# Optimization experiments

Hardware: AMD Instinct MI355X
Metric: run time of the kernel (lower is better)

Reference implementation:

```python
import jax, jax.numpy as jnp
import numpy as np

D_NODE, D_EDGE, D_MODEL, TOPK, N_HEADS = 64, 16, 256, 5, 4
HEAD_DIM = D_MODEL // N_HEADS


def setup_inputs() -> dict:
    key = jax.random.key(0)
    ks = jax.random.split(key, 24)
    B, N = 256, 512
    E = N - 1
    def lin(k, fi, fo):
        k1, k2 = jax.random.split(k)
        s = 1.0 / np.sqrt(fi)
        return (jax.random.uniform(k1, (fi, fo), jnp.float32, -s, s),
                jax.random.uniform(k2, (fo,), jnp.float32, -s, s))
    Wn, bn = lin(ks[0], 8, D_NODE)
    We, be = lin(ks[1], 3, D_EDGE)
    Wq, bq = lin(ks[2], D_NODE, D_MODEL)
    Wkv, bkv = lin(ks[3], 2 * D_NODE + D_EDGE, 2 * D_MODEL)
    # MultiheadAttention in/out projections (fixed shared weights)
    Wiq, biq = lin(ks[4], D_MODEL, D_MODEL)
    Wik, bik = lin(ks[5], D_MODEL, D_MODEL)
    Wiv, biv = lin(ks[6], D_MODEL, D_MODEL)
    Wo, bo = lin(ks[7], D_MODEL, D_MODEL)
    Wf1, bf1 = lin(ks[8], D_NODE + D_MODEL, D_MODEL)
    Wf2, bf2 = lin(ks[9], D_MODEL, D_MODEL)
    Ws1, bs1 = lin(ks[10], D_NODE + D_EDGE + D_MODEL, D_MODEL)
    Ws2, bs2 = lin(ks[11], D_MODEL, 1 + 6 * D_MODEL)
    node_raw = jax.random.normal(ks[12], (B, N, 8), jnp.float32)
    edge_raw = jax.random.normal(ks[13], (B, E, 3), jnp.float32)
    return dict(node_raw=node_raw, edge_raw=edge_raw, ego_id=0,
                Wn=Wn, bn=bn, We=We, be=be, Wq=Wq, bq=bq, Wkv=Wkv, bkv=bkv,
                Wiq=Wiq, biq=biq, Wik=Wik, bik=bik, Wiv=Wiv, biv=biv,
                Wo=Wo, bo=bo, Wf1=Wf1, bf1=bf1, Wf2=Wf2, bf2=bf2,
                Ws1=Ws1, bs1=bs1, Ws2=Ws2, bs2=bs2)


def reference(node_raw, edge_raw, ego_id,
              Wn, bn, We, be, Wq, bq, Wkv, bkv,
              Wiq, biq, Wik, bik, Wiv, biv, Wo, bo,
              Wf1, bf1, Wf2, bf2, Ws1, bs1, Ws2, bs2):
    B, N, _ = node_raw.shape
    E = N - 1
    ego_id = int(ego_id)
    idx = np.arange(N)
    neighbor_idx = jnp.asarray(idx[idx != ego_id])  # (E,)

    node_feat = node_raw @ Wn + bn                   # (B, N, d_node)
    edge_feat = edge_raw @ We + be                   # (B, E, d_edge)
    ego_feat = node_feat[:, ego_id]                  # (B, d_node)
    neighbor_feat = node_feat[:, neighbor_idx]       # (B, E, d_node)

    ego_bcast = jnp.broadcast_to(ego_feat[:, None, :], (B, E, D_NODE))
    edge_input = jnp.concatenate([ego_bcast, edge_feat, neighbor_feat], -1)

    Q = ego_feat @ Wq + bq                           # (B, d_model)
    kv = edge_input @ Wkv + bkv                      # (B, E, 2*d_model)
    K, V = kv[..., :D_MODEL], kv[..., D_MODEL:]

    # MultiheadAttention: single query per batch, E keys/values
    q = (Q @ Wiq + biq).reshape(B, N_HEADS, HEAD_DIM)
    k = (K @ Wik + bik).reshape(B, E, N_HEADS, HEAD_DIM)
    v = (V @ Wiv + biv).reshape(B, E, N_HEADS, HEAD_DIM)
    scores = jnp.einsum('bhd,behd->bhe', q, k) / np.sqrt(HEAD_DIM)
    attn = jax.nn.softmax(scores, axis=-1)           # (B, H, E)
    ctx = jnp.einsum('bhe,behd->bhd', attn, v).reshape(B, D_MODEL)
    c_ego = ctx @ Wo + bo                            # (B, d_model)

    h = jnp.concatenate([ego_feat, c_ego], -1)
    h_ego_prime = jax.nn.relu(h @ Wf1 + bf1) @ Wf2 + bf2  # (B, d_model)

    c_bcast = jnp.broadcast_to(c_ego[:, None, :], (B, E, D_MODEL))
    edge_input2 = jnp.concatenate([neighbor_feat, edge_feat, c_bcast], -1)
    score_out = jax.nn.relu(edge_input2 @ Ws1 + bs1) @ Ws2 + bs2  # (B,E,1+6*dm)
    score = score_out[..., 0]                        # (B, E)
    h_enc = score_out[..., 1:].reshape(B, E, 6, D_MODEL)

    topk_val, topk_idx = jax.lax.top_k(score, TOPK)  # (B, topk)
    selected = jnp.take_along_axis(h_enc, topk_idx[:, :, None, None], axis=1)
    alpha = jax.nn.softmax(topk_val, axis=-1)[:, :, None, None]  # (B,topk,1,1)
    selected = selected * alpha
    return h_ego_prime, selected, topk_idx, alpha
```

## Files before the change

kernel.cpp:

```cpp
#include <hip/hip_runtime.h>
#include <hip/hip_bf16.h>
#include <math.h>

constexpr int B = 256, NN = 512, EE = 511;

constexpr size_t F_NF    = 0;
constexpr size_t F_EF    = F_NF   + (size_t)B*NN*64;
constexpr size_t F_WCK   = F_EF   + (size_t)B*EE*16;
constexpr size_t F_BCK   = F_WCK  + 144*256;
constexpr size_t F_WCV   = F_BCK  + 256;
constexpr size_t F_BCV   = F_WCV  + 144*256;
constexpr size_t F_WQ2   = F_BCV  + 256;
constexpr size_t F_BQ2   = F_WQ2  + 64*256;
constexpr size_t F_Q     = F_BQ2  + 256;
constexpr size_t F_AW    = F_Q    + (size_t)B*256;
constexpr size_t F_C0    = F_AW   + (size_t)B*4*80;
constexpr size_t F_SC    = F_C0   + (size_t)B*4;
constexpr size_t F_US    = F_SC   + (size_t)B*4*EE;
constexpr size_t F_CEGO  = F_US   + (size_t)B*4*80;
constexpr size_t F_CVEC  = F_CEGO + (size_t)B*256;
constexpr size_t F_SC2   = F_CVEC + (size_t)B*256;
constexpr size_t F_ALPHA = F_SC2  + (size_t)B*EE;
constexpr size_t F_TKI   = F_ALPHA+ (size_t)B*5;
constexpr size_t F_HS    = F_SC;

constexpr size_t O_HEGO  = 0;
constexpr size_t O_SEL   = 65536;
constexpr size_t O_TKI   = 2031616;
constexpr size_t O_ALPHA = 2032896;

__global__ void k_fuse(const float* Wkv, const float* bkv, const float* Wik, const float* bik,
                       const float* Wiv, const float* biv, const float* Wq,  const float* bq,
                       const float* Wiq, const float* biq, float* ws){
  int t = blockIdx.x*256 + threadIdx.x;
  if (t < 36864){
    int r = t >> 8, c = t & 255;
    float a = 0.f;
    for (int m=0;m<256;m++) a += Wkv[(size_t)r*512+m] * Wik[(size_t)m*256+c];
    ws[F_WCK + t] = a;
  } else if (t < 37120){
    int c = t - 36864;
    float a = bik[c];
    for (int m=0;m<256;m++) a += bkv[m] * Wik[(size_t)m*256+c];
    ws[F_BCK + c] = a;
  } else if (t < 73984){
    int i = t - 37120; int r = i >> 8, c = i & 255;
    float a = 0.f;
    for (int m=0;m<256;m++) a += Wkv[(size_t)r*512+256+m] * Wiv[(size_t)m*256+c];
    ws[F_WCV + i] = a;
  } else if (t < 74240){
    int c = t - 73984;
    float a = biv[c];
    for (int m=0;m<256;m++) a += bkv[256+m] * Wiv[(size_t)m*256+c];
    ws[F_BCV + c] = a;
  } else if (t < 90624){
    int i = t - 74240; int r = i >> 8, c = i & 255;
    float a = 0.f;
    for (int m=0;m<256;m++) a += Wq[(size_t)r*256+m] * Wiq[(size_t)m*256+c];
    ws[F_WQ2 + i] = a;
  } else if (t < 90880){
    int c = t - 90624;
    float a = biq[c];
    for (int m=0;m<256;m++) a += bq[m] * Wiq[(size_t)m*256+c];
    ws[F_BQ2 + c] = a;
  }
}

__global__ void k_nf(const float* node_raw, const float* Wn, const float* bn, float* ws){
  size_t t = (size_t)blockIdx.x*256 + threadIdx.x;
  int j = (int)(t & 63); size_t row = t >> 6;
  float a = bn[j];
  #pragma unroll
  for (int i=0;i<8;i++) a += node_raw[row*8+i] * Wn[(size_t)i*64+j];
  ws[F_NF + t] = a;
}

__global__ void k_ef(const float* edge_raw, const float* We, const float* be, float* ws){
  size_t t = (size_t)blockIdx.x*256 + threadIdx.x;
  int j = (int)(t & 15); size_t row = t >> 4;
  float a = be[j];
  #pragma unroll
  for (int i=0;i<3;i++) a += edge_raw[row*3+i] * We[(size_t)i*16+j];
  ws[F_EF + t] = a;
}

__global__ void k_head(const int* ego_p, float* ws){
  int b = blockIdx.x >> 2, h = blockIdx.x & 3;
  int tid = threadIdx.x;
  __shared__ float qh[64];
  __shared__ float red[256];
  int ego = *ego_p;
  const float* egf = ws + F_NF + ((size_t)b*NN+ego)*64;
  if (tid < 64){
    int c = h*64 + tid;
    float a = ws[F_BQ2 + c];
    for (int i=0;i<64;i++) a += egf[i]*ws[F_WQ2 + (size_t)i*256 + c];
    qh[tid] = a;
  }
  __syncthreads();
  const float* Wck = ws + F_WCK;
  float p = 0.f;
  size_t awbase = F_AW + ((size_t)(b*4+h))*80;
  if (tid < 64){
    const float* wr = Wck + (size_t)(80+tid)*256 + h*64;
    float a=0.f; for(int d=0;d<64;d++) a += wr[d]*qh[d];
    ws[awbase + tid] = a;
  } else if (tid < 80){
    int i = tid-64;
    const float* wr = Wck + (size_t)(64+i)*256 + h*64;
    float a=0.f; for(int d=0;d<64;d++) a += wr[d]*qh[d];
    ws[awbase + 64 + i] = a;
  } else if (tid < 144){
    int j = tid-80;
    const float* wr = Wck + (size_t)j*256 + h*64;
    float a=0.f; for(int d=0;d<64;d++) a += wr[d]*qh[d];
    p = egf[j] * a;
  } else if (tid < 208){
    int d = tid-144;
    p = ws[F_BCK + h*64 + d] * qh[d];
  }
  red[tid]=p; __syncthreads();
  for (int s=128;s>0;s>>=1){ if(tid<s) red[tid]+=red[tid+s]; __syncthreads(); }
  if (tid==0) ws[F_C0 + b*4 + h] = red[0];
}

__global__ void k_scores(const int* ego_p, float* ws){
  int tile = blockIdx.x, b = blockIdx.y, tid = threadIdx.x;
  __shared__ float awz[4][80];
  __shared__ float c0s[4];
  for (int l=tid; l<320; l+=256) awz[l/80][l%80] = ws[F_AW + (size_t)b*320 + l];
  if (tid<4) c0s[tid] = ws[F_C0 + b*4 + tid];
  __syncthreads();
  int e = tile*256 + tid;
  if (e >= EE) return;
  int ego = *ego_p;
  int node = e < ego ? e : e+1;
  const float4* nr = (const float4*)(ws + F_NF + ((size_t)b*NN+node)*64);
  const float4* er = (const float4*)(ws + F_EF + ((size_t)b*EE+e)*16);
  float s[4] = {c0s[0],c0s[1],c0s[2],c0s[3]};
  #pragma unroll
  for (int i=0;i<16;i++){
    float4 x = nr[i];
    #pragma unroll
    for (int h=0;h<4;h++)
      s[h] += x.x*awz[h][i*4] + x.y*awz[h][i*4+1] + x.z*awz[h][i*4+2] + x.w*awz[h][i*4+3];
  }
  #pragma unroll
  for (int i=0;i<4;i++){
    float4 x = er[i];
    #pragma unroll
    for (int h=0;h<4;h++)
      s[h] += x.x*awz[h][64+i*4] + x.y*awz[h][64+i*4+1] + x.z*awz[h][64+i*4+2] + x.w*awz[h][64+i*4+3];
  }
  #pragma unroll
  for (int h=0;h<4;h++) ws[F_SC + ((size_t)(b*4+h))*EE + e] = s[h]*0.125f;
}

__global__ void k_attn(const int* ego_p, float* ws){
  int bh = blockIdx.x; int b = bh>>2; int tid = threadIdx.x;
  __shared__ float sc[512];
  __shared__ float red[256];
  const float* s = ws + F_SC + (size_t)bh*EE;
  float v0 = tid<EE ? s[tid] : -INFINITY;
  float v1 = (tid+256)<EE ? s[tid+256] : -INFINITY;
  red[tid] = fmaxf(v0,v1); __syncthreads();
  for (int st=128;st>0;st>>=1){ if(tid<st) red[tid]=fmaxf(red[tid],red[tid+st]); __syncthreads(); }
  float m = red[0]; __syncthreads();
  float e0 = tid<EE ? expf(v0-m) : 0.f;
  float e1 = (tid+256)<EE ? expf(v1-m) : 0.f;
  red[tid] = e0+e1; __syncthreads();
  for (int st=128;st>0;st>>=1){ if(tid<st) red[tid]+=red[tid+st]; __syncthreads(); }
  float inv = 1.f/red[0];
  sc[tid] = e0*inv;
  sc[tid+256] = e1*inv;
  __syncthreads();
  int ego = *ego_p;
  if (tid < 64){
    const float* base = ws + F_NF + (size_t)b*NN*64 + tid;
    float a = 0.f;
    for (int e=0;e<EE;e++){
      int node = e<ego?e:e+1;
      a += sc[e]*base[(size_t)node*64];
    }
    ws[F_US + (size_t)bh*80 + tid] = a;
  } else if (tid < 80){
    int d = tid-64;
    const float* base = ws + F_EF + (size_t)b*EE*16 + d;
    float a = 0.f;
    for (int e=0;e<EE;e++) a += sc[e]*base[(size_t)e*16];
    ws[F_US + (size_t)bh*80 + tid] = a;
  }
}

__global__ void k_bfinal(const int* ego_p,
                         const float* Wo, const float* bo,
                         const float* Wf1, const float* bf1p,
                         const float* Wf2, const float* bf2p,
                         const float* Ws1, const float* bs1,
                         float* ws, float* out){
  int b = blockIdx.x, t = threadIdx.x;
  __shared__ float ego_s[64], us_s[4][80], ctx_s[256], cego_s[256], hf_s[256];
  int ego = *ego_p;
  if (t < 64) ego_s[t] = ws[F_NF + ((size_t)b*NN+ego)*64 + t];
  for (int l=t; l<320; l+=256) us_s[l/80][l%80] = ws[F_US + (size_t)b*320 + l];
  __syncthreads();
  {
    int h = t >> 6;
    const float* Wcv = ws + F_WCV;
    float a = ws[F_BCV + t];
    for (int i=0;i<64;i++) a += ego_s[i]*Wcv[(size_t)i*256+t];
    for (int i=0;i<16;i++) a += us_s[h][64+i]*Wcv[(size_t)(64+i)*256+t];
    for (int i=0;i<64;i++) a += us_s[h][i]*Wcv[(size_t)(80+i)*256+t];
    ctx_s[t]=a;
  }
  __syncthreads();
  {
    float a = bo[t];
    for (int i=0;i<256;i++) a += ctx_s[i]*Wo[(size_t)i*256+t];
    cego_s[t]=a; ws[F_CEGO + (size_t)b*256+t]=a;
  }
  __syncthreads();
  {
    float a = bf1p[t];
    for (int i=0;i<64;i++)  a += ego_s[i]*Wf1[(size_t)i*256+t];
    for (int i=0;i<256;i++) a += cego_s[i]*Wf1[(size_t)(64+i)*256+t];
    hf_s[t]=fmaxf(a,0.f);
  }
  __syncthreads();
  {
    float a = bf2p[t];
    for (int i=0;i<256;i++) a += hf_s[i]*Wf2[(size_t)i*256+t];
    out[O_HEGO + (size_t)b*256+t] = a;
  }
  {
    float a = bs1[t];
    for (int i=0;i<256;i++) a += cego_s[i]*Ws1[(size_t)(80+i)*256+t];
    ws[F_CVEC + (size_t)b*256+t]=a;
  }
}

__global__ __launch_bounds__(512) void k_bigscore(const int* ego_p, const float* Ws1,
                                                  const float* Ws2, const float* bs2, float* ws){
  int tile = blockIdx.x, b = blockIdx.y;
  int tid = threadIdx.x;
  __shared__ float Fe[64][80];
  __shared__ float Bs[16][256];
  __shared__ float cv_s[256], w2_s[256];
  int ego = *ego_p;
  if (tid < 256){
    cv_s[tid] = ws[F_CVEC + (size_t)b*256 + tid];
    w2_s[tid] = Ws2[(size_t)tid*1537];
  }
  for (int l=tid; l<80*64; l+=512){
    int e = l/80, k = l - e*80;
    int eg = tile*64 + e;
    float v = 0.f;
    if (eg < EE){
      int node = eg<ego?eg:eg+1;
      v = (k<64) ? ws[F_NF + ((size_t)b*NN+node)*64 + k]
                 : ws[F_EF + ((size_t)b*EE+eg)*16 + (k-64)];
    }
    Fe[e][k] = v;
  }
  int tc = tid & 31, te = tid >> 5;
  float acc[4][8];
  #pragma unroll
  for (int i=0;i<4;i++)
    #pragma unroll
    for (int j=0;j<8;j++) acc[i][j]=0.f;

  for (int c=0;c<5;c++){
    __syncthreads();
    {
      float4* dst = (float4*)&Bs[0][0];
      const float4* s4 = (const float4*)(Ws1 + (size_t)(c*16)*256);
      dst[tid]       = s4[tid];
      dst[tid + 512] = s4[tid + 512];
    }
    __syncthreads();
    #pragma unroll
    for (int kk=0; kk<16; kk+=4){
      float A[4][4];
      #pragma unroll
      for (int i=0;i<4;i++){
        float4 t4 = *(const float4*)&Fe[te*4+i][c*16+kk];
        A[i][0]=t4.x; A[i][1]=t4.y; A[i][2]=t4.z; A[i][3]=t4.w;
      }
      #pragma unroll
      for (int q=0;q<4;q++){
        float4 b0 = *(const float4*)&Bs[kk+q][tc*4];
        float4 b1 = *(const float4*)&Bs[kk+q][128 + tc*4];
        float bw[8] = {b0.x,b0.y,b0.z,b0.w,b1.x,b1.y,b1.z,b1.w};
        #pragma unroll
        for (int i=0;i<4;i++)
          #pragma unroll
          for (int j=0;j<8;j++) acc[i][j] = fmaf(A[i][q], bw[j], acc[i][j]);
      }
    }
  }
  float bs20 = bs2[0];
  #pragma unroll
  for (int i=0;i<4;i++){
    float p = 0.f;
    #pragma unroll
    for (int j=0;j<4;j++){
      int col = tc*4 + j;
      float hcol = acc[i][j] + cv_s[col];
      p += fmaxf(hcol,0.f)*w2_s[col];
    }
    #pragma unroll
    for (int j=0;j<4;j++){
      int col = 128 + tc*4 + j;
      float hcol = acc[i][4+j] + cv_s[col];
      p += fmaxf(hcol,0.f)*w2_s[col];
    }
    #pragma unroll
    for (int m=16;m>0;m>>=1) p += __shfl_xor(p, m, 64);
    if (tc==0){
      int eg = tile*64 + te*4 + i;
      if (eg < EE) ws[F_SC2 + (size_t)b*EE + eg] = p + bs20;
    }
  }
}

__global__ void k_topk(float* ws, float* out){
  int b = blockIdx.x, tid = threadIdx.x;
  __shared__ float sv[256]; __shared__ int si[256];
  __shared__ float tv[8];   __shared__ int tix[8];
  const float* s = ws + F_SC2 + (size_t)b*EE;
  float v0 = tid<EE ? s[tid] : -INFINITY;       int i0 = tid;
  float v1 = (tid+256)<EE ? s[tid+256] : -INFINITY; int i1 = tid+256;
  for (int t=0;t<5;t++){
    float bvv; int bii;
    if (v0 > v1 || (v0==v1 && i0<i1)){ bvv=v0; bii=i0; } else { bvv=v1; bii=i1; }
    sv[tid]=bvv; si[tid]=bii; __syncthreads();
    for (int st=128; st>0; st>>=1){
      if (tid<st){
        float ov=sv[tid+st]; int oi=si[tid+st];
        if (ov > sv[tid] || (ov==sv[tid] && oi<si[tid])){ sv[tid]=ov; si[tid]=oi; }
      }
      __syncthreads();
    }
    if (tid==0){ tv[t]=sv[0]; tix[t]=si[0]; }
    __syncthreads();
    int w = tix[t];
    if (i0==w) v0=-INFINITY;
    if (i1==w) v1=-INFINITY;
    __syncthreads();
  }
  if (tid==0){
    float m = tv[0];
    float ex[5]; float sum=0.f;
    for (int t=0;t<5;t++){ ex[t]=expf(tv[t]-m); sum+=ex[t]; }
    for (int t=0;t<5;t++){
      float al = ex[t]/sum;
      ws[F_ALPHA + (size_t)b*5+t] = al;
      ((int*)(ws + F_TKI))[b*5+t] = tix[t];
      out[O_TKI   + (size_t)b*5+t] = (float)tix[t];
      out[O_ALPHA + (size_t)b*5+t] = al;
    }
  }
}

__global__ void k_hid(const int* ego_p, const float* Ws1, float* ws){
  int bt = blockIdx.x;
  int b = bt/5;
  int tid = threadIdx.x;
  __shared__ float fr[80];
  int e = ((const int*)(ws+F_TKI))[bt];
  int ego = *ego_p;
  int node = e<ego ? e : e+1;
  if (tid < 64)      fr[tid] = ws[F_NF + ((size_t)b*NN+node)*64 + tid];
  else if (tid < 80) fr[tid] = ws[F_EF + ((size_t)b*EE+e)*16 + (tid-64)];
  __syncthreads();
  float a = ws[F_CVEC + (size_t)b*256 + tid];
  for (int d=0;d<80;d++) a += fr[d]*Ws1[(size_t)d*256+tid];
  ws[F_HS + (size_t)bt*256 + tid] = fmaxf(a,0.f);
}

__global__ __launch_bounds__(256) void k_enc(const float* Ws2, const float* bs2,
                                             float* ws, float* out){
  int r = blockIdx.x, g = blockIdx.y, tid = threadIdx.x;
  int n = r*256 + tid;
  __shared__ float hs[10][256];
  __shared__ float al[10];
  int b0 = g*2;
  for (int l=tid; l<10*256; l+=256)
    hs[l>>8][l&255] = ws[F_HS + ((size_t)b0*5)*256 + l];
  if (tid<10) al[tid] = ws[F_ALPHA + (size_t)b0*5 + tid];
  __syncthreads();
  float acc[10];
  #pragma unroll
  for (int i=0;i<10;i++) acc[i]=0.f;
  const float* w2p = Ws2 + 1 + n;
  for (int j=0;j<256;j+=4){
    float w0 = w2p[(size_t)(j+0)*1537];
    float w1 = w2p[(size_t)(j+1)*1537];
    float w2 = w2p[(size_t)(j+2)*1537];
    float w3 = w2p[(size_t)(j+3)*1537];
    #pragma unroll
    for (int i=0;i<10;i++){
      float4 h = *(const float4*)&hs[i][j];
      acc[i] = fmaf(h.x,w0, fmaf(h.y,w1, fmaf(h.z,w2, fmaf(h.w,w3, acc[i]))));
    }
  }
  float bb = bs2[1+n];
  #pragma unroll
  for (int i=0;i<10;i++)
    out[O_SEL + ((size_t)(b0*5+i))*1536 + n] = (acc[i]+bb)*al[i];
}

extern "C" void kernel_launch(void* const* d_in, const int* in_sizes, int n_in,
                              void* d_out, int out_size, void* d_ws, size_t ws_size,
                              hipStream_t stream){
  const float* node_raw=(const float*)d_in[0];
  const float* edge_raw=(const float*)d_in[1];
  const int*  ego_p   =(const int*)d_in[2];
  const float* Wn =(const float*)d_in[3];  const float* bn =(const float*)d_in[4];
  const float* We =(const float*)d_in[5];  const float* be =(const float*)d_in[6];
  const float* Wq =(const float*)d_in[7];  const float* bq =(const float*)d_in[8];
  const float* Wkv=(const float*)d_in[9];  const float* bkv=(const float*)d_in[10];
  const float* Wiq=(const float*)d_in[11]; const float* biq=(const float*)d_in[12];
  const float* Wik=(const float*)d_in[13]; const float* bik=(const float*)d_in[14];
  const float* Wiv=(const float*)d_in[15]; const float* biv=(const float*)d_in[16];
  const float* Wo =(const float*)d_in[17]; const float* bo =(const float*)d_in[18];
  const float* Wf1=(const float*)d_in[19]; const float* bf1p=(const float*)d_in[20];
  const float* Wf2=(const float*)d_in[21]; const float* bf2p=(const float*)d_in[22];
  const float* Ws1=(const float*)d_in[23]; const float* bs1=(const float*)d_in[24];
  const float* Ws2=(const float*)d_in[25]; const float* bs2=(const float*)d_in[26];
  float* ws=(float*)d_ws;
  float* out=(float*)d_out;

  k_fuse<<<355,256,0,stream>>>(Wkv,bkv,Wik,bik,Wiv,biv,Wq,bq,Wiq,biq,ws);
  k_nf<<<(B*NN*64)/256,256,0,stream>>>(node_raw,Wn,bn,ws);
  k_ef<<<(B*EE*16)/256,256,0,stream>>>(edge_raw,We,be,ws);
  k_head<<<B*4,256,0,stream>>>(ego_p,ws);
  k_scores<<<dim3(2,B),256,0,stream>>>(ego_p,ws);
  k_attn<<<B*4,256,0,stream>>>(ego_p,ws);
  k_bfinal<<<B,256,0,stream>>>(ego_p,Wo,bo,Wf1,bf1p,Wf2,bf2p,Ws1,bs1,ws,out);
  k_bigscore<<<dim3(8,B),512,0,stream>>>(ego_p,Ws1,Ws2,bs2,ws);
  k_topk<<<B,256,0,stream>>>(ws,out);
  k_hid<<<B*5,256,0,stream>>>(ego_p,Ws1,ws);
  k_enc<<<dim3(6,128),256,0,stream>>>(Ws2,bs2,ws,out);
}
```

Baseline: 245.7 us.

## Merge node/edge feature kernels and restructure attention pooling per batch

```diff
diff --git a/kernel.cpp b/kernel.cpp
--- a/kernel.cpp
+++ b/kernel.cpp
@@ -66,22 +66,26 @@
   }
 }
 
-__global__ void k_nf(const float* node_raw, const float* Wn, const float* bn, float* ws){
-  size_t t = (size_t)blockIdx.x*256 + threadIdx.x;
-  int j = (int)(t & 63); size_t row = t >> 6;
-  float a = bn[j];
-  #pragma unroll
-  for (int i=0;i<8;i++) a += node_raw[row*8+i] * Wn[(size_t)i*64+j];
-  ws[F_NF + t] = a;
-}
-
-__global__ void k_ef(const float* edge_raw, const float* We, const float* be, float* ws){
-  size_t t = (size_t)blockIdx.x*256 + threadIdx.x;
-  int j = (int)(t & 15); size_t row = t >> 4;
-  float a = be[j];
-  #pragma unroll
-  for (int i=0;i<3;i++) a += edge_raw[row*3+i] * We[(size_t)i*16+j];
-  ws[F_EF + t] = a;
+constexpr int NFB = (B*NN*64)/256;
+constexpr int EFB = (B*EE*16)/256;
+__global__ void k_feat(const float* node_raw, const float* Wn, const float* bn,
+                       const float* edge_raw, const float* We, const float* be, float* ws){
+  int blk = blockIdx.x;
+  if (blk < NFB){
+    size_t t = (size_t)blk*256 + threadIdx.x;
+    int j = (int)(t & 63); size_t row = t >> 6;
+    float a = bn[j];
+    #pragma unroll
+    for (int i=0;i<8;i++) a += node_raw[row*8+i] * Wn[(size_t)i*64+j];
+    ws[F_NF + t] = a;
+  } else {
+    size_t t = (size_t)(blk-NFB)*256 + threadIdx.x;
+    int j = (int)(t & 15); size_t row = t >> 4;
+    float a = be[j];
+    #pragma unroll
+    for (int i=0;i<3;i++) a += edge_raw[row*3+i] * We[(size_t)i*16+j];
+    ws[F_EF + t] = a;
+  }
 }
 
 __global__ void k_head(const int* ego_p, float* ws){
@@ -156,40 +160,66 @@
   for (int h=0;h<4;h++) ws[F_SC + ((size_t)(b*4+h))*EE + e] = s[h]*0.125f;
 }
 
-__global__ void k_attn(const int* ego_p, float* ws){
-  int bh = blockIdx.x; int b = bh>>2; int tid = threadIdx.x;
-  __shared__ float sc[512];
-  __shared__ float red[256];
-  const float* s = ws + F_SC + (size_t)bh*EE;
-  float v0 = tid<EE ? s[tid] : -INFINITY;
-  float v1 = (tid+256)<EE ? s[tid+256] : -INFINITY;
-  red[tid] = fmaxf(v0,v1); __syncthreads();
-  for (int st=128;st>0;st>>=1){ if(tid<st) red[tid]=fmaxf(red[tid],red[tid+st]); __syncthreads(); }
-  float m = red[0]; __syncthreads();
-  float e0 = tid<EE ? expf(v0-m) : 0.f;
-  float e1 = (tid+256)<EE ? expf(v1-m) : 0.f;
-  red[tid] = e0+e1; __syncthreads();
-  for (int st=128;st>0;st>>=1){ if(tid<st) red[tid]+=red[tid+st]; __syncthreads(); }
-  float inv = 1.f/red[0];
-  sc[tid] = e0*inv;
-  sc[tid+256] = e1*inv;
-  __syncthreads();
-  int ego = *ego_p;
-  if (tid < 64){
-    const float* base = ws + F_NF + (size_t)b*NN*64 + tid;
-    float a = 0.f;
-    for (int e=0;e<EE;e++){
-      int node = e<ego?e:e+1;
-      a += sc[e]*base[(size_t)node*64];
-    }
-    ws[F_US + (size_t)bh*80 + tid] = a;
-  } else if (tid < 80){
-    int d = tid-64;
-    const float* base = ws + F_EF + (size_t)b*EE*16 + d;
-    float a = 0.f;
-    for (int e=0;e<EE;e++) a += sc[e]*base[(size_t)e*16];
-    ws[F_US + (size_t)bh*80 + tid] = a;
-  }
+__global__ __launch_bounds__(256) void k_attn(const int* ego_p, float* ws){
+  int b = blockIdx.x, tid = threadIdx.x;
+  int h = tid >> 6, lane = tid & 63;
+  __shared__ float sc[4][512];
+  __shared__ float tnf[32][64];
+  __shared__ float tef[32][16];
+  const float* s = ws + F_SC + ((size_t)(b*4+h))*EE;
+  float v[8];
+  float mx = -INFINITY;
+  #pragma unroll
+  for (int j=0;j<8;j++){
+    int e = lane + j*64;
+    v[j] = (e<EE) ? s[e] : -INFINITY;
+    mx = fmaxf(mx, v[j]);
+  }
+  #pragma unroll
+  for (int m=32;m>0;m>>=1) mx = fmaxf(mx, __shfl_xor(mx, m, 64));
+  float sum = 0.f;
+  #pragma unroll
+  for (int j=0;j<8;j++){
+    int e = lane + j*64;
+    float ev = (e<EE) ? expf(v[j]-mx) : 0.f;
+    v[j] = ev; sum += ev;
+  }
+  #pragma unroll
+  for (int m=32;m>0;m>>=1) sum += __shfl_xor(sum, m, 64);
+  float inv = 1.f/sum;
+  #pragma unroll
+  for (int j=0;j<8;j++) sc[h][lane + j*64] = v[j]*inv;
+  __syncthreads();
+  int ego = *ego_p;
+  float accn = 0.f;
+  float acce = 0.f;
+  for (int t0=0; t0<EE; t0+=32){
+    __syncthreads();
+    for (int q=tid; q<512; q+=256){
+      int e = t0 + (q>>4), c4 = q & 15;
+      float4 val = make_float4(0.f,0.f,0.f,0.f);
+      if (e < EE){
+        int node = e<ego ? e : e+1;
+        val = *(const float4*)(ws + F_NF + ((size_t)b*NN+node)*64 + c4*4);
+      }
+      *(float4*)&tnf[q>>4][c4*4] = val;
+    }
+    if (tid < 128){
+      int e = t0 + (tid>>2), c4 = tid & 3;
+      float4 val = make_float4(0.f,0.f,0.f,0.f);
+      if (e < EE) val = *(const float4*)(ws + F_EF + ((size_t)b*EE+e)*16 + c4*4);
+      *(float4*)&tef[tid>>2][c4*4] = val;
+    }
+    __syncthreads();
+    #pragma unroll 8
+    for (int e=0;e<32;e++){
+      float a = sc[h][t0+e];
+      accn = fmaf(a, tnf[e][lane], accn);
+      if (lane < 16) acce = fmaf(a, tef[e][lane], acce);
+    }
+  }
+  ws[F_US + ((size_t)(b*4+h))*80 + lane] = accn;
+  if (lane < 16) ws[F_US + ((size_t)(b*4+h))*80 + 64 + lane] = acce;
 }
 
 __global__ void k_bfinal(const int* ego_p,
@@ -432,11 +462,10 @@
   float* out=(float*)d_out;
 
   k_fuse<<<355,256,0,stream>>>(Wkv,bkv,Wik,bik,Wiv,biv,Wq,bq,Wiq,biq,ws);
-  k_nf<<<(B*NN*64)/256,256,0,stream>>>(node_raw,Wn,bn,ws);
-  k_ef<<<(B*EE*16)/256,256,0,stream>>>(edge_raw,We,be,ws);
+  k_feat<<<NFB+EFB,256,0,stream>>>(node_raw,Wn,bn,edge_raw,We,be,ws);
   k_head<<<B*4,256,0,stream>>>(ego_p,ws);
   k_scores<<<dim3(2,B),256,0,stream>>>(ego_p,ws);
-  k_attn<<<B*4,256,0,stream>>>(ego_p,ws);
+  k_attn<<<B,256,0,stream>>>(ego_p,ws);
   k_bfinal<<<B,256,0,stream>>>(ego_p,Wo,bo,Wf1,bf1p,Wf2,bf2p,Ws1,bs1,ws,out);
   k_bigscore<<<dim3(8,B),512,0,stream>>>(ego_p,Ws1,Ws2,bs2,ws);
   k_topk<<<B,256,0,stream>>>(ws,out);
```

New measurement: 251.6 us. 1.02x slower.

## Split k_fuse reduction across threads, read Ws1 directly in bigscore, drop unused store

Applied to the files above, without the earlier changes.

```diff
diff --git a/kernel.cpp b/kernel.cpp
--- a/kernel.cpp
+++ b/kernel.cpp
@@ -29,40 +29,44 @@
 constexpr size_t O_TKI   = 2031616;
 constexpr size_t O_ALPHA = 2032896;
 
-__global__ void k_fuse(const float* Wkv, const float* bkv, const float* Wik, const float* bik,
+__global__ __launch_bounds__(256) void k_fuse(const float* Wkv, const float* bkv,
+                       const float* Wik, const float* bik,
                        const float* Wiv, const float* biv, const float* Wq,  const float* bq,
                        const float* Wiq, const float* biq, float* ws){
-  int t = blockIdx.x*256 + threadIdx.x;
-  if (t < 36864){
-    int r = t >> 8, c = t & 255;
-    float a = 0.f;
-    for (int m=0;m<256;m++) a += Wkv[(size_t)r*512+m] * Wik[(size_t)m*256+c];
-    ws[F_WCK + t] = a;
-  } else if (t < 37120){
-    int c = t - 36864;
-    float a = bik[c];
-    for (int m=0;m<256;m++) a += bkv[m] * Wik[(size_t)m*256+c];
-    ws[F_BCK + c] = a;
-  } else if (t < 73984){
-    int i = t - 37120; int r = i >> 8, c = i & 255;
-    float a = 0.f;
-    for (int m=0;m<256;m++) a += Wkv[(size_t)r*512+256+m] * Wiv[(size_t)m*256+c];
-    ws[F_WCV + i] = a;
-  } else if (t < 74240){
-    int c = t - 73984;
-    float a = biv[c];
-    for (int m=0;m<256;m++) a += bkv[256+m] * Wiv[(size_t)m*256+c];
-    ws[F_BCV + c] = a;
-  } else if (t < 90624){
-    int i = t - 74240; int r = i >> 8, c = i & 255;
-    float a = 0.f;
-    for (int m=0;m<256;m++) a += Wq[(size_t)r*256+m] * Wiq[(size_t)m*256+c];
-    ws[F_WQ2 + i] = a;
-  } else if (t < 90880){
-    int c = t - 90624;
-    float a = biq[c];
-    for (int m=0;m<256;m++) a += bq[m] * Wiq[(size_t)m*256+c];
-    ws[F_BQ2 + c] = a;
+  int o = threadIdx.x & 63, ks = threadIdx.x >> 6;
+  int g = blockIdx.x*64 + o;
+  int m0 = ks*64;
+  float a = 0.f;
+  if (g < 36864){
+    int r = g >> 8, c = g & 255;
+    for (int m=m0; m<m0+64; m++) a += Wkv[(size_t)r*512+m] * Wik[(size_t)m*256+c];
+  } else if (g < 37120){
+    int c = g - 36864;
+    for (int m=m0; m<m0+64; m++) a += bkv[m] * Wik[(size_t)m*256+c];
+  } else if (g < 73984){
+    int i = g - 37120; int r = i >> 8, c = i & 255;
+    for (int m=m0; m<m0+64; m++) a += Wkv[(size_t)r*512+256+m] * Wiv[(size_t)m*256+c];
+  } else if (g < 74240){
+    int c = g - 73984;
+    for (int m=m0; m<m0+64; m++) a += bkv[256+m] * Wiv[(size_t)m*256+c];
+  } else if (g < 90624){
+    int i = g - 74240; int r = i >> 8, c = i & 255;
+    for (int m=m0; m<m0+64; m++) a += Wq[(size_t)r*256+m] * Wiq[(size_t)m*256+c];
+  } else if (g < 90880){
+    int c = g - 90624;
+    for (int m=m0; m<m0+64; m++) a += bq[m] * Wiq[(size_t)m*256+c];
+  }
+  __shared__ float red[256];
+  red[threadIdx.x] = a;
+  __syncthreads();
+  if (ks == 0 && g < 90880){
+    float s = red[o] + red[64+o] + red[128+o] + red[192+o];
+    if (g < 36864)      ws[F_WCK + g] = s;
+    else if (g < 37120) ws[F_BCK + (g-36864)] = s + bik[g-36864];
+    else if (g < 73984) ws[F_WCV + (g-37120)] = s;
+    else if (g < 74240) ws[F_BCV + (g-73984)] = s + biv[g-73984];
+    else if (g < 90624) ws[F_WQ2 + (g-74240)] = s;
+    else                ws[F_BQ2 + (g-90624)] = s + biq[g-90624];
   }
 }
 
@@ -217,7 +221,7 @@
   {
     float a = bo[t];
     for (int i=0;i<256;i++) a += ctx_s[i]*Wo[(size_t)i*256+t];
-    cego_s[t]=a; ws[F_CEGO + (size_t)b*256+t]=a;
+    cego_s[t]=a;
   }
   __syncthreads();
   {
@@ -244,7 +248,6 @@
   int tile = blockIdx.x, b = blockIdx.y;
   int tid = threadIdx.x;
   __shared__ float Fe[64][80];
-  __shared__ float Bs[16][256];
   __shared__ float cv_s[256], w2_s[256];
   int ego = *ego_p;
   if (tid < 256){
@@ -262,6 +265,7 @@
     }
     Fe[e][k] = v;
   }
+  __syncthreads();
   int tc = tid & 31, te = tid >> 5;
   float acc[4][8];
   #pragma unroll
@@ -269,33 +273,22 @@
     #pragma unroll
     for (int j=0;j<8;j++) acc[i][j]=0.f;
 
-  for (int c=0;c<5;c++){
-    __syncthreads();
-    {
-      float4* dst = (float4*)&Bs[0][0];
-      const float4* s4 = (const float4*)(Ws1 + (size_t)(c*16)*256);
-      dst[tid]       = s4[tid];
-      dst[tid + 512] = s4[tid + 512];
-    }
-    __syncthreads();
-    #pragma unroll
-    for (int kk=0; kk<16; kk+=4){
-      float A[4][4];
+  for (int kk=0; kk<80; kk+=4){
+    float A[4][4];
+    #pragma unroll
+    for (int i=0;i<4;i++){
+      float4 t4 = *(const float4*)&Fe[te*4+i][kk];
+      A[i][0]=t4.x; A[i][1]=t4.y; A[i][2]=t4.z; A[i][3]=t4.w;
+    }
+    #pragma unroll
+    for (int q=0;q<4;q++){
+      float4 b0 = *(const float4*)(Ws1 + (size_t)(kk+q)*256 + tc*4);
+      float4 b1 = *(const float4*)(Ws1 + (size_t)(kk+q)*256 + 128 + tc*4);
+      float bw[8] = {b0.x,b0.y,b0.z,b0.w,b1.x,b1.y,b1.z,b1.w};
       #pragma unroll
-      for (int i=0;i<4;i++){
-        float4 t4 = *(const float4*)&Fe[te*4+i][c*16+kk];
-        A[i][0]=t4.x; A[i][1]=t4.y; A[i][2]=t4.z; A[i][3]=t4.w;
-      }
-      #pragma unroll
-      for (int q=0;q<4;q++){
-        float4 b0 = *(const float4*)&Bs[kk+q][tc*4];
-        float4 b1 = *(const float4*)&Bs[kk+q][128 + tc*4];
-        float bw[8] = {b0.x,b0.y,b0.z,b0.w,b1.x,b1.y,b1.z,b1.w};
+      for (int i=0;i<4;i++)
         #pragma unroll
-        for (int i=0;i<4;i++)
-          #pragma unroll
-          for (int j=0;j<8;j++) acc[i][j] = fmaf(A[i][q], bw[j], acc[i][j]);
-      }
+        for (int j=0;j<8;j++) acc[i][j] = fmaf(A[i][q], bw[j], acc[i][j]);
     }
   }
   float bs20 = bs2[0];
@@ -431,7 +424,7 @@
   float* ws=(float*)d_ws;
   float* out=(float*)d_out;
 
-  k_fuse<<<355,256,0,stream>>>(Wkv,bkv,Wik,bik,Wiv,biv,Wq,bq,Wiq,biq,ws);
+  k_fuse<<<1420,256,0,stream>>>(Wkv,bkv,Wik,bik,Wiv,biv,Wq,bq,Wiq,biq,ws);
   k_nf<<<(B*NN*64)/256,256,0,stream>>>(node_raw,Wn,bn,ws);
   k_ef<<<(B*EE*16)/256,256,0,stream>>>(edge_raw,We,be,ws);
   k_head<<<B*4,256,0,stream>>>(ego_p,ws);
```

New measurement: 267.8 us. +9.0%, slower.
